# Kernel tuning notes

Measured on AMD Instinct MI355X. Metric: run time of the kernel, lower is better.

The kernel has to match this reference:

```python
import jax, jax.numpy as jnp
import numpy as np

NUM_HEADS = 4

def setup_inputs() -> dict:
    key = jax.random.key(0)
    ks = jax.random.split(key, 5)
    B, N, C = 2, 4096, 256
    s = 0.02
    return {
        "x": jax.random.normal(ks[0], (B, N, C), dtype=jnp.float32),
        "qkv_w": jax.random.normal(ks[1], (3 * C, C), dtype=jnp.float32) * s,
        "qkv_b": jax.random.normal(ks[2], (3 * C,), dtype=jnp.float32) * s,
        "out_w": jax.random.normal(ks[3], (C, C), dtype=jnp.float32) * s,
        "out_b": jax.random.normal(ks[4], (C,), dtype=jnp.float32) * s,
    }

def reference(x, qkv_w, qkv_b, out_w, out_b):
    # x: [B, N, C]; manual multi-head self-attention (eval mode, dropout off)
    B, N, C = x.shape
    H = NUM_HEADS
    D = C // H
    qkv = x @ qkv_w.T + qkv_b                      # [B, N, 3C]
    qkv = qkv.reshape(B, N, 3, H, D)
    qkv = jnp.transpose(qkv, (2, 0, 3, 1, 4))      # [3, B, H, N, D]
    q, k, v = qkv[0], qkv[1], qkv[2]
    scale = D ** -0.5
    attn = jnp.einsum('bhnd,bhmd->bhnm', q, k) * scale  # [B, H, N, N]
    attn = jax.nn.softmax(attn, axis=-1)
    out = jnp.einsum('bhnm,bhmd->bhnd', attn, v)   # [B, H, N, D]
    out = jnp.transpose(out, (0, 2, 1, 3)).reshape(B, N, C)
    return out @ out_w.T + out_b
```

## Files before the change

### kernel.cpp

```cpp
#include <hip/hip_runtime.h>

typedef __bf16 bf16x8 __attribute__((ext_vector_type(8)));
typedef float f32x4 __attribute__((ext_vector_type(4)));

#define MFMA_BF16(a, b, c) __builtin_amdgcn_mfma_f32_16x16x32_bf16((a), (b), (c), 0, 0, 0)

#define C1 0.18033688f

static __device__ __forceinline__ unsigned short f2bf(float f) {
    unsigned int u = __float_as_uint(f);
    unsigned int r = (u + 0x7fffu + ((u >> 16) & 1u)) >> 16;
    return (unsigned short)r;
}
static __device__ __forceinline__ float bf2f(unsigned short us) {
    return __uint_as_float(((unsigned int)us) << 16);
}
static __device__ __forceinline__ float exp2_hw(float x) {
    float r;
    asm("v_exp_f32 %0, %1" : "=v"(r) : "v"(x));
    return r;
}
static __device__ __forceinline__ unsigned pack_rh(float a, float b) {
    return __byte_perm(__float_as_uint(a) + 0x8000u, __float_as_uint(b) + 0x8000u, 0x7632);
}
static __device__ __forceinline__ void gload16(const void* g, void* l) {
    __builtin_amdgcn_global_load_lds(
        (const __attribute__((address_space(1))) unsigned int*)g,
        (__attribute__((address_space(3))) unsigned int*)l, 16, 0, 0);
}

static __device__ __forceinline__ void conv_seg(const void* src, unsigned short* dst, int n,
                                                int lb, bool f32) {
#pragma unroll
    for (int j = 0; j < 4; j++) {
        int idx = lb * 1024 + j * 256 + (int)threadIdx.x;
        if (idx < n) {
            dst[idx] = f32 ? f2bf(((const float*)src)[idx]) : ((const unsigned short*)src)[idx];
        }
    }
}

__global__ __launch_bounds__(256) void convert_kernel(
    const void* __restrict__ x, const void* __restrict__ qw, const void* __restrict__ qb,
    const void* __restrict__ ow, const void* __restrict__ ob,
    unsigned short* __restrict__ xb, unsigned short* __restrict__ qwb,
    unsigned short* __restrict__ qbb, unsigned short* __restrict__ owb,
    unsigned short* __restrict__ obb, int* __restrict__ flag) {
    __shared__ int tot;
    if (threadIdx.x == 0) tot = 0;
    __syncthreads();
    {
        unsigned short v = ((const unsigned short*)x)[threadIdx.x];
        int e = (v >> 7) & 0xFF;
        if (e >= 195) atomicAdd(&tot, 1);
    }
    __syncthreads();
    const bool f32 = (tot >= 8);
    if (blockIdx.x == 0 && threadIdx.x == 0) flag[0] = f32 ? 1 : 0;

    const int bid = blockIdx.x;
    if (bid < 2048)       conv_seg(x,  xb,  2097152, bid,        f32);
    else if (bid < 2240)  conv_seg(qw, qwb, 196608,  bid - 2048, f32);
    else if (bid < 2241)  conv_seg(qb, qbb, 768,     bid - 2240, f32);
    else if (bid < 2305)  conv_seg(ow, owb, 65536,   bid - 2241, f32);
    else                  conv_seg(ob, obb, 256,     bid - 2305, f32);
}

template <int BM, bool QKV>
__global__ __launch_bounds__(256) void gemm_kernel(
    const unsigned short* __restrict__ A, const unsigned short* __restrict__ W,
    const unsigned short* __restrict__ bias, unsigned short* __restrict__ Cb,
    float* __restrict__ Cf, const int* __restrict__ flag,
    unsigned short* __restrict__ Vt, int Nout) {
    constexpr int K = 256;
    constexpr int WPM = BM / 64;
    constexpr int IA = BM / 32;
    constexpr int ABYT = BM * 128;
    __shared__ __align__(16) char sm[2 * ABYT + 16384];

    const int tid = threadIdx.x;
    const int lane = tid & 63;
    const int wv = tid >> 6;
    const int m16 = lane & 15;
    const int quad = lane >> 4;
    const int bm = blockIdx.x * BM;
    const int bn = blockIdx.y * 64;

    int ago[IA], alo[IA];
#pragma unroll
    for (int i = 0; i < IA; i++) {
        const int c = wv * (IA * 64) + i * 64 + lane;
        const int r = c >> 3, g = (c & 7) ^ (r & 7);
        ago[i] = r * (K * 2) + g * 16;
        alo[i] = c * 16;
    }
    int bgo[2], blo[2];
#pragma unroll
    for (int i = 0; i < 2; i++) {
        const int c = wv * 128 + i * 64 + lane;
        const int r = c >> 3, g = (c & 7) ^ (r & 7);
        bgo[i] = r * (K * 2) + g * 16;
        blo[i] = c * 16;
    }
    int aro[WPM][2], bro[4][2];
#pragma unroll
    for (int mb = 0; mb < WPM; mb++)
#pragma unroll
        for (int ks = 0; ks < 2; ks++) {
            const int row = wv * (WPM * 16) + mb * 16 + m16;
            aro[mb][ks] = row * 64 + ((4 * ks + quad) ^ (m16 & 7)) * 8;
        }
#pragma unroll
    for (int t = 0; t < 4; t++)
#pragma unroll
        for (int ks = 0; ks < 2; ks++) {
            const int row = t * 16 + m16;
            bro[t][ks] = row * 64 + ((4 * ks + quad) ^ (m16 & 7)) * 8;
        }

    const char* ag = (const char*)(A + (size_t)bm * K);
    const char* bg = (const char*)(W + (size_t)bn * K);

#pragma unroll
    for (int i = 0; i < IA; i++) gload16(ag + ago[i], sm + alo[i]);
#pragma unroll
    for (int i = 0; i < 2; i++) gload16(bg + bgo[i], sm + 2 * ABYT + blo[i]);

    f32x4 acc[WPM][4] = {};
#pragma unroll
    for (int kb = 0; kb < 4; kb++) {
        __syncthreads();
        const int cur = kb & 1;
        if (kb < 3) {
            ag += 128;
            bg += 128;
            char* Adst = sm + (cur ^ 1) * ABYT;
            char* Bdst = sm + 2 * ABYT + (cur ^ 1) * 8192;
#pragma unroll
            for (int i = 0; i < IA; i++) gload16(ag + ago[i], Adst + alo[i]);
#pragma unroll
            for (int i = 0; i < 2; i++) gload16(bg + bgo[i], Bdst + blo[i]);
        }
        const unsigned short* Alds = (const unsigned short*)(sm + cur * ABYT);
        const unsigned short* Blds = (const unsigned short*)(sm + 2 * ABYT + cur * 8192);
#pragma unroll
        for (int ks = 0; ks < 2; ks++) {
            bf16x8 bfr[4];
#pragma unroll
            for (int t = 0; t < 4; t++) bfr[t] = *(const bf16x8*)(Blds + bro[t][ks]);
#pragma unroll
            for (int mb = 0; mb < WPM; mb++) {
                const bf16x8 af = *(const bf16x8*)(Alds + aro[mb][ks]);
#pragma unroll
                for (int t = 0; t < 4; t++) acc[mb][t] = MFMA_BF16(af, bfr[t], acc[mb][t]);
            }
        }
    }

    const bool outf = (!QKV) && (flag != nullptr) && (*flag != 0);
#pragma unroll
    for (int mb = 0; mb < WPM; mb++) {
        const int row0 = bm + wv * (WPM * 16) + mb * 16 + quad * 4;
#pragma unroll
        for (int t = 0; t < 4; t++) {
            const int col = bn + t * 16 + m16;
            const float bv = bf2f(bias[col]);
            float v[4];
#pragma unroll
            for (int r = 0; r < 4; r++) v[r] = acc[mb][t][r] + bv;
            if (QKV) {
                if (col < 256) {
#pragma unroll
                    for (int r = 0; r < 4; r++)
                        Cb[(size_t)(row0 + r) * 768 + col] = f2bf(v[r] * C1);
                } else if (col < 512) {
#pragma unroll
                    for (int r = 0; r < 4; r++)
                        Cb[(size_t)(row0 + r) * 768 + col] = f2bf(v[r]);
                } else {
                    const int hh = (col - 512) >> 6, d = (col - 512) & 63;
                    const int bb = row0 >> 12, n0 = row0 & 4095;
                    uint2 w2;
                    w2.x = pack_rh(v[0], v[1]);
                    w2.y = pack_rh(v[2], v[3]);
                    *(uint2*)&Vt[((size_t)((bb * 4 + hh) * 64 + d)) * 4096 + n0] = w2;
                }
            } else {
                if (outf) {
#pragma unroll
                    for (int r = 0; r < 4; r++) Cf[(size_t)(row0 + r) * Nout + col] = v[r];
                } else {
#pragma unroll
                    for (int r = 0; r < 4; r++) Cb[(size_t)(row0 + r) * Nout + col] = f2bf(v[r]);
                }
            }
        }
    }
}

__global__ __launch_bounds__(256) void attn_kernel(
    const unsigned short* __restrict__ qkv, const unsigned short* __restrict__ Vt,
    unsigned short* __restrict__ attn, int iters) {
    const int N = 4096, C3 = 768;
    __shared__ __align__(16) char sm[65536];

    const int tid = threadIdx.x;
    const int lane = tid & 63;
    const int wv = tid >> 6;
    const int m16 = lane & 15;
    const int quad = lane >> 4;

    const int bh = blockIdx.x & 7;
    const int qt = blockIdx.x >> 3;
    const int b = bh >> 2, h = bh & 3;

    bf16x8 qf[4][2];
#pragma unroll
    for (int j = 0; j < 4; j++)
#pragma unroll
        for (int ks = 0; ks < 2; ks++)
            qf[j][ks] = *(const bf16x8*)(qkv + ((size_t)b * N + qt * 64 + j * 16 + m16) * C3 +
                                         h * 64 + ks * 32 + quad * 8);

    uint4 ones_u;
    ones_u.x = ones_u.y = ones_u.z = ones_u.w = 0x3F803F80u;
    const bf16x8 ones = *(const bf16x8*)&ones_u;

    int kgo[4], vgo[4], klo[4], vlo[4];
#pragma unroll
    for (int i = 0; i < 4; i++) {
        const int c = wv * 256 + i * 64 + lane;
        const int r = c >> 3, g = (c & 7) ^ (r & 7);
        kgo[i] = r * 1536 + g * 16;
        klo[i] = c * 16;
        const int d = c >> 4, gg = (c & 15) ^ (d & 15);
        vgo[i] = d * 8192 + gg * 16;
        vlo[i] = c * 16;
    }
    int kro[2][2], vro[4], pwo[2][4], pro[4];
#pragma unroll
    for (int mb = 0; mb < 2; mb++)
#pragma unroll
        for (int ks = 0; ks < 2; ks++) {
            const int row = wv * 32 + mb * 16 + m16;
            kro[mb][ks] = row * 64 + ((4 * ks + quad) ^ (m16 & 7)) * 8;
        }
#pragma unroll
    for (int t = 0; t < 4; t++) vro[t] = (t * 16 + m16) * 128 + ((wv * 4 + quad) ^ m16) * 8;
#pragma unroll
    for (int mb = 0; mb < 2; mb++)
#pragma unroll
        for (int j = 0; j < 4; j++)
            pwo[mb][j] = wv * 2048 + (j * 16 + m16) * 32 +
                         ((2 * mb + (quad >> 1)) ^ (m16 & 3)) * 8 + (quad & 1) * 4;
#pragma unroll
    for (int j = 0; j < 4; j++)
        pro[j] = wv * 2048 + (j * 16 + m16) * 32 + (quad ^ (m16 & 3)) * 8;

    const char* kgp = (const char*)(qkv + (size_t)b * N * C3 + 256 + h * 64);
    const char* vgp = (const char*)(Vt + (size_t)bh * 64 * N);

#pragma unroll
    for (int i = 0; i < 4; i++) {
        gload16(kgp + kgo[i], sm + klo[i]);
        gload16(vgp + vgo[i], sm + 32768 + vlo[i]);
    }

    f32x4 o[4][4] = {};
    f32x4 o1[4] = {};

    for (int kt = 0; kt < iters; ++kt) {
        __syncthreads();
        const int cur = kt & 1;
        if (kt + 1 < iters) {
            kgp += 128 * 1536;
            vgp += 256;
            char* Kdst = sm + (cur ^ 1) * 16384;
            char* Vdst = sm + 32768 + (cur ^ 1) * 16384;
#pragma unroll
            for (int i = 0; i < 4; i++) {
                gload16(kgp + kgo[i], Kdst + klo[i]);
                gload16(vgp + vgo[i], Vdst + vlo[i]);
            }
        }
        unsigned short* Kb = (unsigned short*)(sm + cur * 16384);
        const unsigned short* Vb = (const unsigned short*)(sm + 32768 + cur * 16384);

        f32x4 s[2][4] = {};
#pragma unroll
        for (int mb = 0; mb < 2; mb++)
#pragma unroll
            for (int ks = 0; ks < 2; ks++) {
                const bf16x8 ka = *(const bf16x8*)(Kb + kro[mb][ks]);
#pragma unroll
                for (int j = 0; j < 4; j++) s[mb][j] = MFMA_BF16(ka, qf[j][ks], s[mb][j]);
            }

#pragma unroll
        for (int mb = 0; mb < 2; mb++)
#pragma unroll
            for (int j = 0; j < 4; j++) {
                const float p0 = exp2_hw(s[mb][j][0]);
                const float p1 = exp2_hw(s[mb][j][1]);
                const float p2 = exp2_hw(s[mb][j][2]);
                const float p3 = exp2_hw(s[mb][j][3]);
                uint2 w;
                w.x = pack_rh(p0, p1);
                w.y = pack_rh(p2, p3);
                *(uint2*)(Kb + pwo[mb][j]) = w;
            }
        asm volatile("s_waitcnt lgkmcnt(0)" ::: "memory");

        bf16x8 pa[4];
#pragma unroll
        for (int j = 0; j < 4; j++) pa[j] = *(const bf16x8*)(Kb + pro[j]);
#pragma unroll
        for (int j = 0; j < 4; j++) o1[j] = MFMA_BF16(pa[j], ones, o1[j]);
#pragma unroll
        for (int t = 0; t < 4; t++) {
            const bf16x8 vb = *(const bf16x8*)(Vb + vro[t]);
#pragma unroll
            for (int j = 0; j < 4; j++) o[j][t] = MFMA_BF16(pa[j], vb, o[j][t]);
        }
    }

    __syncthreads();
    float* Ored = (float*)sm;
    float* lsum = (float*)(sm + 16384);
    if (m16 == 0) {
#pragma unroll
        for (int j = 0; j < 4; j++)
#pragma unroll
            for (int r = 0; r < 4; r++)
                lsum[wv * 64 + j * 16 + quad * 4 + r] = o1[j][r];
    }
    const int row = tid >> 4;
    const int col = (tid & 15) * 4;
#pragma unroll
    for (int j = 0; j < 4; j++) {
#pragma unroll
        for (int t = 0; t < 4; t++)
#pragma unroll
            for (int r = 0; r < 4; r++)
                Ored[(wv * 16 + quad * 4 + r) * 64 + t * 16 + m16] = o[j][t][r];
        __syncthreads();
        f32x4 sum = *(f32x4*)&Ored[row * 64 + col];
        sum += *(f32x4*)&Ored[1024 + row * 64 + col];
        sum += *(f32x4*)&Ored[2048 + row * 64 + col];
        sum += *(f32x4*)&Ored[3072 + row * 64 + col];
        const float lq = lsum[j * 16 + row] + lsum[64 + j * 16 + row] +
                         lsum[128 + j * 16 + row] + lsum[192 + j * 16 + row];
        const int n = qt * 64 + j * 16 + row;
        const float inv = 1.0f / lq;
        uint2 w;
        w.x = pack_rh(sum[0] * inv, sum[1] * inv);
        w.y = pack_rh(sum[2] * inv, sum[3] * inv);
        *(uint2*)&attn[((size_t)b * N + n) * 256 + h * 64 + col] = w;
        __syncthreads();
    }
}

extern "C" void kernel_launch(void* const* d_in, const int* in_sizes, int n_in,
                              void* d_out, int out_size, void* d_ws, size_t ws_size,
                              hipStream_t stream) {
    const int B = 2, N = 4096, H = 4;
    const int M = B * N;

    char* wsb = (char*)d_ws;
    int* flag = (int*)wsb;
    unsigned short* xb      = (unsigned short*)(wsb + 64);
    unsigned short* qwb     = xb + 2097152;
    unsigned short* qbb     = qwb + 196608;
    unsigned short* owb     = qbb + 768;
    unsigned short* obb     = owb + 65536;
    unsigned short* qkv_ws  = obb + 256;
    unsigned short* Vt_ws   = qkv_ws + 6291456;
    unsigned short* attn_ws = Vt_ws + 2097152;

    convert_kernel<<<2306, 256, 0, stream>>>(d_in[0], d_in[1], d_in[2], d_in[3], d_in[4],
                                             xb, qwb, qbb, owb, obb, flag);

    gemm_kernel<128, true><<<dim3(M / 128, 768 / 64), 256, 0, stream>>>(
        xb, qwb, qbb, qkv_ws, nullptr, nullptr, Vt_ws, 768);

    attn_kernel<<<512, 256, 0, stream>>>(qkv_ws, Vt_ws, attn_ws, 32);

    gemm_kernel<64, false><<<dim3(M / 64, 256 / 64), 256, 0, stream>>>(
        attn_ws, owb, obb, (unsigned short*)d_out, (float*)d_out, flag, nullptr, 256);
}
```

Before: 146.6 us.

## Vectorize input conversion, load GEMM A operand directly, coalesce V transpose via LDS

The convert kernel now handles 8 elements per thread, using 16-byte vector loads and stores with packed bf16 rounding, so it launches half as many blocks. The GEMM drops the LDS staging of the A operand. Each wave reads its A fragments straight from global memory into registers and prefetches the next K block, while only W stays double-buffered in LDS. The QKV GEMM tile shrinks to 64 rows, and the V-part output is transposed through LDS so the Vt writes become full 16-byte coalesced rows. This cuts LDS traffic and scattered 8-byte stores, at the cost of more blocks and direct global A reads. The bf16 rounding switches to pack_rh (round-half-up), which is slightly different from round-to-nearest-even.

```diff
diff --git a/kernel.cpp b/kernel.cpp
--- a/kernel.cpp
+++ b/kernel.cpp
@@ -29,13 +29,21 @@
         (__attribute__((address_space(3))) unsigned int*)l, 16, 0, 0);
 }
 
-static __device__ __forceinline__ void conv_seg(const void* src, unsigned short* dst, int n,
-                                                int lb, bool f32) {
-#pragma unroll
-    for (int j = 0; j < 4; j++) {
-        int idx = lb * 1024 + j * 256 + (int)threadIdx.x;
-        if (idx < n) {
-            dst[idx] = f32 ? f2bf(((const float*)src)[idx]) : ((const unsigned short*)src)[idx];
+static __device__ __forceinline__ void conv_seg8(const void* src, unsigned short* dst, int n,
+                                                 int lb, bool f32) {
+    const int base = lb * 2048 + (int)threadIdx.x * 8;
+    if (base < n) {
+        if (f32) {
+            const float4 u0 = *(const float4*)((const float*)src + base);
+            const float4 u1 = *(const float4*)((const float*)src + base + 4);
+            uint4 p;
+            p.x = pack_rh(u0.x, u0.y);
+            p.y = pack_rh(u0.z, u0.w);
+            p.z = pack_rh(u1.x, u1.y);
+            p.w = pack_rh(u1.z, u1.w);
+            *(uint4*)(dst + base) = p;
+        } else {
+            *(uint4*)(dst + base) = *(const uint4*)((const unsigned short*)src + base);
         }
     }
 }
@@ -59,41 +67,30 @@
     if (blockIdx.x == 0 && threadIdx.x == 0) flag[0] = f32 ? 1 : 0;
 
     const int bid = blockIdx.x;
-    if (bid < 2048)       conv_seg(x,  xb,  2097152, bid,        f32);
-    else if (bid < 2240)  conv_seg(qw, qwb, 196608,  bid - 2048, f32);
-    else if (bid < 2241)  conv_seg(qb, qbb, 768,     bid - 2240, f32);
-    else if (bid < 2305)  conv_seg(ow, owb, 65536,   bid - 2241, f32);
-    else                  conv_seg(ob, obb, 256,     bid - 2305, f32);
-}
-
-template <int BM, bool QKV>
+    if (bid < 1024)       conv_seg8(x,  xb,  2097152, bid,        f32);
+    else if (bid < 1120)  conv_seg8(qw, qwb, 196608,  bid - 1024, f32);
+    else if (bid < 1121)  conv_seg8(qb, qbb, 768,     bid - 1120, f32);
+    else if (bid < 1153)  conv_seg8(ow, owb, 65536,   bid - 1121, f32);
+    else                  conv_seg8(ob, obb, 256,     bid - 1153, f32);
+}
+
+template <bool QKV>
 __global__ __launch_bounds__(256) void gemm_kernel(
     const unsigned short* __restrict__ A, const unsigned short* __restrict__ W,
     const unsigned short* __restrict__ bias, unsigned short* __restrict__ Cb,
     float* __restrict__ Cf, const int* __restrict__ flag,
     unsigned short* __restrict__ Vt, int Nout) {
     constexpr int K = 256;
-    constexpr int WPM = BM / 64;
-    constexpr int IA = BM / 32;
-    constexpr int ABYT = BM * 128;
-    __shared__ __align__(16) char sm[2 * ABYT + 16384];
+    __shared__ __align__(16) char sm[16384];
 
     const int tid = threadIdx.x;
     const int lane = tid & 63;
     const int wv = tid >> 6;
     const int m16 = lane & 15;
     const int quad = lane >> 4;
-    const int bm = blockIdx.x * BM;
+    const int bm = blockIdx.x * 64;
     const int bn = blockIdx.y * 64;
 
-    int ago[IA], alo[IA];
-#pragma unroll
-    for (int i = 0; i < IA; i++) {
-        const int c = wv * (IA * 64) + i * 64 + lane;
-        const int r = c >> 3, g = (c & 7) ^ (r & 7);
-        ago[i] = r * (K * 2) + g * 16;
-        alo[i] = c * 16;
-    }
     int bgo[2], blo[2];
 #pragma unroll
     for (int i = 0; i < 2; i++) {
@@ -102,14 +99,7 @@
         bgo[i] = r * (K * 2) + g * 16;
         blo[i] = c * 16;
     }
-    int aro[WPM][2], bro[4][2];
-#pragma unroll
-    for (int mb = 0; mb < WPM; mb++)
-#pragma unroll
-        for (int ks = 0; ks < 2; ks++) {
-            const int row = wv * (WPM * 16) + mb * 16 + m16;
-            aro[mb][ks] = row * 64 + ((4 * ks + quad) ^ (m16 & 7)) * 8;
-        }
+    int bro[4][2];
 #pragma unroll
     for (int t = 0; t < 4; t++)
 #pragma unroll
@@ -118,81 +108,90 @@
             bro[t][ks] = row * 64 + ((4 * ks + quad) ^ (m16 & 7)) * 8;
         }
 
-    const char* ag = (const char*)(A + (size_t)bm * K);
     const char* bg = (const char*)(W + (size_t)bn * K);
-
-#pragma unroll
-    for (int i = 0; i < IA; i++) gload16(ag + ago[i], sm + alo[i]);
-#pragma unroll
-    for (int i = 0; i < 2; i++) gload16(bg + bgo[i], sm + 2 * ABYT + blo[i]);
-
-    f32x4 acc[WPM][4] = {};
+    const unsigned short* ap = A + (size_t)(bm + wv * 16 + m16) * K + quad * 8;
+
+#pragma unroll
+    for (int i = 0; i < 2; i++) gload16(bg + bgo[i], sm + blo[i]);
+    bf16x8 a0 = *(const bf16x8*)(ap);
+    bf16x8 a1 = *(const bf16x8*)(ap + 32);
+
+    f32x4 acc[4] = {};
 #pragma unroll
     for (int kb = 0; kb < 4; kb++) {
         __syncthreads();
         const int cur = kb & 1;
+        bf16x8 a0n, a1n;
         if (kb < 3) {
-            ag += 128;
             bg += 128;
-            char* Adst = sm + (cur ^ 1) * ABYT;
-            char* Bdst = sm + 2 * ABYT + (cur ^ 1) * 8192;
-#pragma unroll
-            for (int i = 0; i < IA; i++) gload16(ag + ago[i], Adst + alo[i]);
+            char* Bdst = sm + (cur ^ 1) * 8192;
 #pragma unroll
             for (int i = 0; i < 2; i++) gload16(bg + bgo[i], Bdst + blo[i]);
-        }
-        const unsigned short* Alds = (const unsigned short*)(sm + cur * ABYT);
-        const unsigned short* Blds = (const unsigned short*)(sm + 2 * ABYT + cur * 8192);
+            a0n = *(const bf16x8*)(ap + (kb + 1) * 64);
+            a1n = *(const bf16x8*)(ap + (kb + 1) * 64 + 32);
+        }
+        const unsigned short* Blds = (const unsigned short*)(sm + cur * 8192);
 #pragma unroll
         for (int ks = 0; ks < 2; ks++) {
-            bf16x8 bfr[4];
-#pragma unroll
-            for (int t = 0; t < 4; t++) bfr[t] = *(const bf16x8*)(Blds + bro[t][ks]);
-#pragma unroll
-            for (int mb = 0; mb < WPM; mb++) {
-                const bf16x8 af = *(const bf16x8*)(Alds + aro[mb][ks]);
-#pragma unroll
-                for (int t = 0; t < 4; t++) acc[mb][t] = MFMA_BF16(af, bfr[t], acc[mb][t]);
-            }
-        }
+            const bf16x8 a = ks ? a1 : a0;
+#pragma unroll
+            for (int t = 0; t < 4; t++) {
+                const bf16x8 b = *(const bf16x8*)(Blds + bro[t][ks]);
+                acc[t] = MFMA_BF16(a, b, acc[t]);
+            }
+        }
+        if (kb < 3) {
+            a0 = a0n;
+            a1 = a1n;
+        }
+    }
+
+    if (QKV && bn >= 512) {
+        __syncthreads();
+        unsigned short* tr = (unsigned short*)sm;
+        const int lr = wv * 16 + quad * 4;
+#pragma unroll
+        for (int t = 0; t < 4; t++) {
+            const float bv = bf2f(bias[bn + t * 16 + m16]);
+            uint2 w;
+            w.x = pack_rh(acc[t][0] + bv, acc[t][1] + bv);
+            w.y = pack_rh(acc[t][2] + bv, acc[t][3] + bv);
+            *(uint2*)&tr[(t * 16 + m16) * 72 + lr] = w;
+        }
+        __syncthreads();
+        const int d = tid >> 2;
+        const int ch = (tid & 3) * 16;
+        const uint4 o4a = *(const uint4*)&tr[d * 72 + ch];
+        const uint4 o4b = *(const uint4*)&tr[d * 72 + ch + 8];
+        const int hh = (bn - 512) >> 6;
+        const int bb = bm >> 12, n0 = bm & 4095;
+        unsigned short* vdst = &Vt[((size_t)((bb * 4 + hh) * 64 + d)) * 4096 + n0 + ch];
+        *(uint4*)(vdst) = o4a;
+        *(uint4*)(vdst + 8) = o4b;
+        return;
     }
 
     const bool outf = (!QKV) && (flag != nullptr) && (*flag != 0);
-#pragma unroll
-    for (int mb = 0; mb < WPM; mb++) {
-        const int row0 = bm + wv * (WPM * 16) + mb * 16 + quad * 4;
-#pragma unroll
-        for (int t = 0; t < 4; t++) {
-            const int col = bn + t * 16 + m16;
-            const float bv = bf2f(bias[col]);
-            float v[4];
-#pragma unroll
-            for (int r = 0; r < 4; r++) v[r] = acc[mb][t][r] + bv;
-            if (QKV) {
-                if (col < 256) {
-#pragma unroll
-                    for (int r = 0; r < 4; r++)
-                        Cb[(size_t)(row0 + r) * 768 + col] = f2bf(v[r] * C1);
-                } else if (col < 512) {
-#pragma unroll
-                    for (int r = 0; r < 4; r++)
-                        Cb[(size_t)(row0 + r) * 768 + col] = f2bf(v[r]);
-                } else {
-                    const int hh = (col - 512) >> 6, d = (col - 512) & 63;
-                    const int bb = row0 >> 12, n0 = row0 & 4095;
-                    uint2 w2;
-                    w2.x = pack_rh(v[0], v[1]);
-                    w2.y = pack_rh(v[2], v[3]);
-                    *(uint2*)&Vt[((size_t)((bb * 4 + hh) * 64 + d)) * 4096 + n0] = w2;
-                }
+    const int row0 = bm + wv * 16 + quad * 4;
+#pragma unroll
+    for (int t = 0; t < 4; t++) {
+        const int col = bn + t * 16 + m16;
+        const float bv = bf2f(bias[col]);
+        float v[4];
+#pragma unroll
+        for (int r = 0; r < 4; r++) v[r] = acc[t][r] + bv;
+        if (QKV) {
+            const float sc = (col < 256) ? C1 : 1.0f;
+#pragma unroll
+            for (int r = 0; r < 4; r++)
+                Cb[(size_t)(row0 + r) * 768 + col] = f2bf(v[r] * sc);
+        } else {
+            if (outf) {
+#pragma unroll
+                for (int r = 0; r < 4; r++) Cf[(size_t)(row0 + r) * Nout + col] = v[r];
             } else {
-                if (outf) {
-#pragma unroll
-                    for (int r = 0; r < 4; r++) Cf[(size_t)(row0 + r) * Nout + col] = v[r];
-                } else {
-#pragma unroll
-                    for (int r = 0; r < 4; r++) Cb[(size_t)(row0 + r) * Nout + col] = f2bf(v[r]);
-                }
+#pragma unroll
+                for (int r = 0; r < 4; r++) Cb[(size_t)(row0 + r) * Nout + col] = f2bf(v[r]);
             }
         }
     }
@@ -377,14 +376,14 @@
     unsigned short* Vt_ws   = qkv_ws + 6291456;
     unsigned short* attn_ws = Vt_ws + 2097152;
 
-    convert_kernel<<<2306, 256, 0, stream>>>(d_in[0], d_in[1], d_in[2], d_in[3], d_in[4],
+    convert_kernel<<<1154, 256, 0, stream>>>(d_in[0], d_in[1], d_in[2], d_in[3], d_in[4],
                                              xb, qwb, qbb, owb, obb, flag);
 
-    gemm_kernel<128, true><<<dim3(M / 128, 768 / 64), 256, 0, stream>>>(
+    gemm_kernel<true><<<dim3(M / 64, 768 / 64), 256, 0, stream>>>(
         xb, qwb, qbb, qkv_ws, nullptr, nullptr, Vt_ws, 768);
 
     attn_kernel<<<512, 256, 0, stream>>>(qkv_ws, Vt_ws, attn_ws, 32);
 
-    gemm_kernel<64, false><<<dim3(M / 64, 256 / 64), 256, 0, stream>>>(
+    gemm_kernel<false><<<dim3(M / 64, 256 / 64), 256, 0, stream>>>(
         attn_ws, owb, obb, (unsigned short*)d_out, (float*)d_out, flag, nullptr, 256);
 }
```

After: 144.8 us. No clear change (-1.2%).
